# Kernel tuning notes

Hardware: AMD Instinct MI355X
Metric: run time of the kernel (lower is better)

Reference implementation:

```python
import jax, jax.numpy as jnp
import numpy as np
import math

B, N, D, H = 2, 64, 256, 8
DK = D // H


def setup_inputs() -> dict:
    key = jax.random.key(0)
    ks = jax.random.split(key, 12)
    s = 1.0 / math.sqrt(D)
    inp = {
        "state": jax.random.normal(ks[0], (B, N, N, D), dtype=jnp.float32),
        "mask": jnp.zeros((B, N, N, N), dtype=bool),
        "W_lk": jax.random.normal(ks[1], (D, D), dtype=jnp.float32) * s,
        "b_lk": jnp.zeros((D,), dtype=jnp.float32),
        "W_rk": jax.random.normal(ks[2], (D, D), dtype=jnp.float32) * s,
        "b_rk": jnp.zeros((D,), dtype=jnp.float32),
        "W_lv": jax.random.normal(ks[3], (D, D), dtype=jnp.float32) * s,
        "b_lv": jnp.zeros((D,), dtype=jnp.float32),
        "W_rv": jax.random.normal(ks[4], (D, D), dtype=jnp.float32) * s,
        "b_rv": jnp.zeros((D,), dtype=jnp.float32),
        "W_o": jax.random.normal(ks[5], (D, D), dtype=jnp.float32) * s,
        "b_o": jnp.zeros((D,), dtype=jnp.float32),
    }
    return inp


def _proj(x, W, b):
    # torch nn.Linear: x @ W.T + b, then view to heads
    y = jnp.einsum('bxyd,ed->bxye', x, W) + b
    return y.reshape(B, N, N, H, DK)


def reference(state, mask, W_lk, b_lk, W_rk, b_rk, W_lv, b_lv, W_rv, b_rv, W_o, b_o):
    left_k = _proj(state, W_lk, b_lk)   # [B,N,N,H,DK]
    right_k = _proj(state, W_rk, b_rk)
    left_v = _proj(state, W_lv, b_lv)
    right_v = _proj(state, W_rv, b_rv)

    # triangle-style scores over node triples (x, a, y): [B,N,N,N,H]
    scores = jnp.einsum('bxahd,bayhd->bxayh', left_k, right_k) / math.sqrt(DK)
    scores = jnp.where(mask[..., None], jnp.float32(-1000.0), scores)
    att = jax.nn.softmax(scores, axis=2)  # softmax over intermediate node a

    # val[b,x,a,y,h,d] = left_v[b,x,a,h,d] * right_v[b,a,y,h,d] (materialized as in torch)
    val = jnp.einsum('bxahd,bayhd->bxayhd', left_v, right_v)
    x = jnp.einsum('bxayh,bxayhd->bxyhd', att, val)  # sum over a
    x = x.reshape(B, N, N, D)
    return jnp.einsum('bxyd,ed->bxye', x, W_o) + b_o
```

## Files before the change

kernel.cpp:

```cpp
#include <hip/hip_runtime.h>

#define B 2
#define N 64
#define D 256
#define H 8
#define DK 32
#define M (B * N * N)

typedef __attribute__((ext_vector_type(8))) short bf16x8;
typedef __attribute__((ext_vector_type(4))) float f32x4;
typedef __attribute__((ext_vector_type(2))) float f32x2;

#define PROJ_ELEMS (2097152)

__device__ __forceinline__ ushort f2b(float f) {
    union { float f; unsigned u; } v; v.f = f;
    unsigned r = v.u + 0x7fffu + ((v.u >> 16) & 1u);
    return (ushort)(r >> 16);
}
__device__ __forceinline__ float b2f(ushort u) {
    union { unsigned u; float f; } v; v.u = ((unsigned)u) << 16; return v.f;
}
__device__ __forceinline__ f32x2 up2(unsigned u) {
    union { unsigned u; float f; } lo, hi;
    lo.u = u << 16; hi.u = u & 0xffff0000u;
    f32x2 r; r.x = lo.f; r.y = hi.f; return r;
}

__device__ __forceinline__ void glds16(const ushort* g, ushort* l) {
    __builtin_amdgcn_global_load_lds(
        (const __attribute__((address_space(1))) unsigned int*)g,
        (__attribute__((address_space(3))) unsigned int*)l, 16, 0, 0);
}

__global__ __launch_bounds__(256) void cast_all(const float* __restrict__ state,
                                                const float* __restrict__ W_lk, const float* __restrict__ W_rk,
                                                const float* __restrict__ W_lv, const float* __restrict__ W_rv,
                                                const float* __restrict__ W_o,
                                                const float* __restrict__ b_lk, const float* __restrict__ b_rk,
                                                const float* __restrict__ b_lv, const float* __restrict__ b_rv,
                                                const float* __restrict__ b_o,
                                                ushort* __restrict__ state_bf,
                                                ushort* __restrict__ Wcat,
                                                float* __restrict__ bias_cat) {
    const int gid = blockIdx.x * 256 + threadIdx.x;
    const float* Ws[5] = {W_lk, W_rk, W_lv, W_rv, W_o};
    const float* bs[5] = {b_lk, b_rk, b_lv, b_rv, b_o};

    if (gid < 1280) bias_cat[gid] = bs[gid >> 8][gid & 255];

    if (gid < 524288) {
        float4 v = *(const float4*)&state[(size_t)gid * 4];
        ushort4 o = {f2b(v.x), f2b(v.y), f2b(v.z), f2b(v.w)};
        *(ushort4*)&state_bf[(size_t)gid * 4] = o;
    } else {
        int u = gid - 524288;
        int row = u >> 6;
        int k4 = (u & 63) * 4;
        const float* W = Ws[row >> 8];
        float4 v = *(const float4*)&W[(size_t)(row & 255) * 256 + k4];
        ushort4 o = {f2b(v.x), f2b(v.y), f2b(v.z), f2b(v.w)};
        *(ushort4*)&Wcat[(size_t)row * 256 + k4] = o;
    }
}

template <int BF16OUT, int RELAYOUT, int BM>
__global__ __launch_bounds__(256) void gemm_mfma(const ushort* __restrict__ A,
                                                 const ushort* __restrict__ Bw,
                                                 const float* __restrict__ bias,
                                                 void* __restrict__ Cv, int ldc) {
    constexpr int IR = BM / 32;
    __shared__ __align__(16) ushort As[2][2][BM * 32];
    __shared__ __align__(16) ushort Bs[2][2][128 * 32];
    const int tid = threadIdx.x;
    const int lane = tid & 63;
    const int wave = tid >> 6;
    const int wm = (wave & 1) * (BM / 2);
    const int wn = (wave >> 1) * 64;
    const int row0 = blockIdx.x * BM;
    const int col0 = blockIdx.y * 128;

    const int lr = lane >> 2;
    const int lkq = (lane & 3) * 8;

    const int arow = (BM == 128) ? (wave * 32) : (wave * 16);
    const ushort* gA0 = A + (size_t)(row0 + arow + lr) * 256 + lkq;
    const ushort* gA1 = gA0 + 16 * 256;
    const ushort* gB0 = Bw + (size_t)(col0 + wave * 32 + lr) * 256 + lkq;
    const ushort* gB1 = gB0 + 16 * 256;

    const int fr = lane & 15;
    const int fk = (lane >> 4) * 8;

    f32x4 acc[IR][4] = {};

    auto stage2 = [&](int grp) {
        const int buf = grp & 1;
#pragma unroll
        for (int p = 0; p < 2; ++p) {
            const int ko = (grp * 2 + p) * 32;
            glds16(gA0 + ko, &As[buf][p][arow * 32]);
            if (BM == 128) glds16(gA1 + ko, &As[buf][p][(arow + 16) * 32]);
            glds16(gB0 + ko, &Bs[buf][p][(wave * 32) * 32]);
            glds16(gB1 + ko, &Bs[buf][p][(wave * 32 + 16) * 32]);
        }
    };

    stage2(0);
    __syncthreads();

    for (int it = 0; it < 4; ++it) {
        if (it < 3) stage2(it + 1);
        const int buf = it & 1;
#pragma unroll
        for (int p = 0; p < 2; ++p) {
            bf16x8 af[IR], bf[4];
#pragma unroll
            for (int i = 0; i < IR; ++i)
                af[i] = *(const bf16x8*)&As[buf][p][(wm + i * 16 + fr) * 32 + fk];
#pragma unroll
            for (int j = 0; j < 4; ++j)
                bf[j] = *(const bf16x8*)&Bs[buf][p][(wn + j * 16 + fr) * 32 + fk];
#pragma unroll
            for (int i = 0; i < IR; ++i)
#pragma unroll
                for (int j = 0; j < 4; ++j)
                    acc[i][j] = __builtin_amdgcn_mfma_f32_16x16x32_bf16(af[i], bf[j], acc[i][j], 0, 0, 0);
        }
        __syncthreads();
    }

#pragma unroll
    for (int j = 0; j < 4; ++j) {
        const int col = col0 + wn + j * 16 + (lane & 15);
        const float bv = bias[col];
#pragma unroll
        for (int i = 0; i < IR; ++i) {
            const int rbase = row0 + wm + i * 16 + (lane >> 4) * 4;
#pragma unroll
            for (int r = 0; r < 4; ++r) {
                float o = acc[i][j][r] + bv;
                if (RELAYOUT) {
                    const int row = rbase + r;
                    const int bb = row >> 12, rr = row & 4095;
                    const int proj = col >> 8, hh = (col >> 5) & 7, dk = col & 31;
                    ((ushort*)Cv)[(size_t)proj * PROJ_ELEMS +
                                  ((size_t)(bb * 8 + hh) * 4096 + rr) * 32 + dk] = f2b(o);
                } else if (BF16OUT) {
                    ((ushort*)Cv)[(size_t)(rbase + r) * ldc + col] = f2b(o);
                } else {
                    ((float*)Cv)[(size_t)(rbase + r) * ldc + col] = o;
                }
            }
        }
    }
}

__global__ __launch_bounds__(512, 2) void fused_attn(const ushort* __restrict__ P,
                                                     const unsigned char* __restrict__ mask,
                                                     ushort* __restrict__ xbuf) {
    __shared__ __align__(16) ushort LVb[16 * 1024];
    __shared__ __align__(16) ushort RVb[32 * 512];
    __shared__ __align__(16) float atts[32 * 16 * 20];
    __shared__ float mstate[16 * 20];
    __shared__ float alphas[16 * 20];

    const int bh = blockIdx.z;
    const int b = bh >> 3, h = bh & 7;
    const int x0 = blockIdx.x * 16, y0 = blockIdx.y * 16;
    const int tid = threadIdx.x;
    const int lane = tid & 63, wave = tid >> 6;

    const size_t HB = (size_t)bh * 4096 * 32;
    const ushort* PLK = P + HB;
    const ushort* PRK = P + (size_t)1 * PROJ_ELEMS + HB;
    const ushort* PLV = P + (size_t)2 * PROJ_ELEMS + HB;
    const ushort* PRV = P + (size_t)3 * PROJ_ELEMS + HB;

    const int gy = lane >> 2;
    const int du = lane & 3;
    const int sx = tid >> 4, sy = tid & 15;
    if (tid < 256) mstate[sx * 20 + sy] = -3.0e38f;

    const int sa = lane >> 2, soct = lane & 3;
    const int r2 = wave * 2;
    const int a4 = wave * 4;

    f32x2 acc[2][4] = {};
    float lacc[2] = {0.0f, 0.0f};
    const float scale = 0.17677669529663687f;

    for (int c = 0; c < 2; ++c) {
        const int ac = c * 32;
        __syncthreads();

        glds16(PLV + ((size_t)(x0 + r2) * 64 + ac + sa) * 32 + soct * 8,
               &LVb[r2 * 1024]);
        glds16(PLV + ((size_t)(x0 + r2) * 64 + ac + 16 + sa) * 32 + soct * 8,
               &LVb[r2 * 1024 + 512]);
        glds16(PLV + ((size_t)(x0 + r2 + 1) * 64 + ac + sa) * 32 + soct * 8,
               &LVb[(r2 + 1) * 1024]);
        glds16(PLV + ((size_t)(x0 + r2 + 1) * 64 + ac + 16 + sa) * 32 + soct * 8,
               &LVb[(r2 + 1) * 1024 + 512]);
#pragma unroll
        for (int k = 0; k < 4; ++k)
            glds16(PRV + ((size_t)(ac + a4 + k) * 64 + y0 + sa) * 32 + soct * 8,
                   &RVb[(a4 + k) * 512]);

        {
            const int fr = lane & 15, fk = (lane >> 4) * 8;
            const int yq = lane & 15, xq = (lane >> 4) * 4;
#pragma unroll
            for (int aw = 0; aw < 4; ++aw) {
                const int a = wave * 4 + aw;
                bf16x8 af = *(const bf16x8*)&PLK[((size_t)(x0 + fr) * 64 + ac + a) * 32 + fk];
                bf16x8 bf = *(const bf16x8*)&PRK[((size_t)(ac + a) * 64 + y0 + fr) * 32 + fk];
                f32x4 s = {};
                s = __builtin_amdgcn_mfma_f32_16x16x32_bf16(af, bf, s, 0, 0, 0);
#pragma unroll
                for (int rr = 0; rr < 4; ++rr) {
                    const int x = xq + rr;
                    float sv = s[rr] * scale;
                    if (mask[((size_t)(b * N + x0 + x) * N + ac + a) * N + y0 + yq]) sv = -1000.0f;
                    atts[(a * 16 + x) * 20 + yq] = sv;
                }
            }
        }
        __syncthreads();

        if (tid < 256) {
            float mc = -3.0e38f;
#pragma unroll
            for (int a = 0; a < 32; ++a) mc = fmaxf(mc, atts[(a * 16 + sx) * 20 + sy]);
            const float mold = mstate[sx * 20 + sy];
            const float mnew = fmaxf(mold, mc);
            mstate[sx * 20 + sy] = mnew;
            alphas[sx * 20 + sy] = __expf(mold - mnew);
        }
        __syncthreads();

        float mn[2];
#pragma unroll
        for (int i = 0; i < 2; ++i) {
            const int x = wave * 2 + i;
            const float av = alphas[x * 20 + gy];
            mn[i] = mstate[x * 20 + gy];
            lacc[i] *= av;
#pragma unroll
            for (int q = 0; q < 4; ++q) acc[i][q] *= av;
        }

        {
            const unsigned* LV32 = (const unsigned*)LVb;
            const unsigned* RV32 = (const unsigned*)RVb;
#pragma unroll
            for (int a = 0; a < 32; ++a) {
                const uint4 rvw = *(const uint4*)&RV32[a * 256 + gy * 16 + du * 4];
                const f32x2 rv0 = up2(rvw.x), rv1 = up2(rvw.y);
                const f32x2 rv2 = up2(rvw.z), rv3 = up2(rvw.w);
#pragma unroll
                for (int i = 0; i < 2; ++i) {
                    const int x = wave * 2 + i;
                    const uint4 lvw = *(const uint4*)&LV32[x * 512 + a * 16 + du * 4];
                    const float sv = atts[(a * 16 + x) * 20 + gy];
                    const float w = __expf(sv - mn[i]);
                    lacc[i] += w;
                    acc[i][0] += (up2(lvw.x) * w) * rv0;
                    acc[i][1] += (up2(lvw.y) * w) * rv1;
                    acc[i][2] += (up2(lvw.z) * w) * rv2;
                    acc[i][3] += (up2(lvw.w) * w) * rv3;
                }
            }
        }
    }

#pragma unroll
    for (int i = 0; i < 2; ++i) {
        const int x = wave * 2 + i;
        const float il = 1.0f / lacc[i];
        ushort o[8] __attribute__((aligned(16)));
#pragma unroll
        for (int q = 0; q < 4; ++q) {
            o[2 * q]     = f2b(acc[i][q].x * il);
            o[2 * q + 1] = f2b(acc[i][q].y * il);
        }
        *(uint4*)&xbuf[(((size_t)b * N + x0 + x) * N + y0 + gy) * D + h * DK + du * 8] =
            *(const uint4*)o;
    }
}

extern "C" void kernel_launch(void* const* d_in, const int* in_sizes, int n_in,
                              void* d_out, int out_size, void* d_ws, size_t ws_size,
                              hipStream_t stream) {
    const float* state = (const float*)d_in[0];
    const unsigned char* mask = (const unsigned char*)d_in[1];
    const float* W_lk = (const float*)d_in[2];
    const float* b_lk = (const float*)d_in[3];
    const float* W_rk = (const float*)d_in[4];
    const float* b_rk = (const float*)d_in[5];
    const float* W_lv = (const float*)d_in[6];
    const float* b_lv = (const float*)d_in[7];
    const float* W_rv = (const float*)d_in[8];
    const float* b_rv = (const float*)d_in[9];
    const float* W_o = (const float*)d_in[10];
    const float* b_o = (const float*)d_in[11];
    float* out = (float*)d_out;

    char* ws = (char*)d_ws;
    ushort* P_bf = (ushort*)ws;
    ws += (size_t)4 * PROJ_ELEMS * 2;
    float* bias_cat = (float*)ws;
    ws += 1280 * 4;
    ushort* state_bf = (ushort*)ws;
    ws += (size_t)M * D * 2;
    ushort* Wcat = (ushort*)ws;
    ws += (size_t)1280 * 256 * 2;
    ushort* xbuf_bf = (ushort*)ws;

    cast_all<<<2368, 256, 0, stream>>>(state, W_lk, W_rk, W_lv, W_rv, W_o,
                                       b_lk, b_rk, b_lv, b_rv, b_o,
                                       state_bf, Wcat, bias_cat);
    gemm_mfma<1, 1, 128><<<dim3(M / 128, 8), 256, 0, stream>>>(state_bf, Wcat, bias_cat, P_bf, 1024);
    fused_attn<<<dim3(4, 4, B * H), 512, 0, stream>>>(P_bf, mask, xbuf_bf);
    gemm_mfma<0, 0, 64><<<dim3(M / 64, 2), 256, 0, stream>>>(xbuf_bf, Wcat + 1024 * 256, bias_cat + 1024, out, 256);
}
```

Measured before the change: 124.0 us.

## Load left values directly into registers with prefetch and transpose score tile

Drops the shared-memory staging buffer for left values. Each thread now reads its own left-value rows from global memory into registers, with a four-deep software prefetch inside the accumulation loop. The score tile in shared memory is transposed so the MFMA output is stored as one float4, and the two per-thread weights are read as a float2. This cuts LDS traffic and footprint, which may raise occupancy, but the accumulation loop now depends on global load latency and more registers are in use.

```diff
diff --git a/kernel.cpp b/kernel.cpp
--- a/kernel.cpp
+++ b/kernel.cpp
@@ -159,7 +159,6 @@
 __global__ __launch_bounds__(512, 2) void fused_attn(const ushort* __restrict__ P,
                                                      const unsigned char* __restrict__ mask,
                                                      ushort* __restrict__ xbuf) {
-    __shared__ __align__(16) ushort LVb[16 * 1024];
     __shared__ __align__(16) ushort RVb[32 * 512];
     __shared__ __align__(16) float atts[32 * 16 * 20];
     __shared__ float mstate[16 * 20];
@@ -183,8 +182,10 @@
     if (tid < 256) mstate[sx * 20 + sy] = -3.0e38f;
 
     const int sa = lane >> 2, soct = lane & 3;
-    const int r2 = wave * 2;
     const int a4 = wave * 4;
+
+    const ushort* lvb0 = PLV + ((size_t)(x0 + wave * 2) * 64) * 32 + du * 8;
+    const ushort* lvb1 = lvb0 + 64 * 32;
 
     f32x2 acc[2][4] = {};
     float lacc[2] = {0.0f, 0.0f};
@@ -194,18 +195,17 @@
         const int ac = c * 32;
         __syncthreads();
 
-        glds16(PLV + ((size_t)(x0 + r2) * 64 + ac + sa) * 32 + soct * 8,
-               &LVb[r2 * 1024]);
-        glds16(PLV + ((size_t)(x0 + r2) * 64 + ac + 16 + sa) * 32 + soct * 8,
-               &LVb[r2 * 1024 + 512]);
-        glds16(PLV + ((size_t)(x0 + r2 + 1) * 64 + ac + sa) * 32 + soct * 8,
-               &LVb[(r2 + 1) * 1024]);
-        glds16(PLV + ((size_t)(x0 + r2 + 1) * 64 + ac + 16 + sa) * 32 + soct * 8,
-               &LVb[(r2 + 1) * 1024 + 512]);
 #pragma unroll
         for (int k = 0; k < 4; ++k)
             glds16(PRV + ((size_t)(ac + a4 + k) * 64 + y0 + sa) * 32 + soct * 8,
                    &RVb[(a4 + k) * 512]);
+
+        uint4 lvp[4][2];
+#pragma unroll
+        for (int s = 0; s < 4; ++s) {
+            lvp[s][0] = *(const uint4*)(lvb0 + (ac + s) * 32);
+            lvp[s][1] = *(const uint4*)(lvb1 + (ac + s) * 32);
+        }
 
         {
             const int fr = lane & 15, fk = (lane >> 4) * 8;
@@ -217,13 +217,16 @@
                 bf16x8 bf = *(const bf16x8*)&PRK[((size_t)(ac + a) * 64 + y0 + fr) * 32 + fk];
                 f32x4 s = {};
                 s = __builtin_amdgcn_mfma_f32_16x16x32_bf16(af, bf, s, 0, 0, 0);
+                float4 ov;
+                float* op = (float*)&ov;
 #pragma unroll
                 for (int rr = 0; rr < 4; ++rr) {
-                    const int x = xq + rr;
                     float sv = s[rr] * scale;
-                    if (mask[((size_t)(b * N + x0 + x) * N + ac + a) * N + y0 + yq]) sv = -1000.0f;
-                    atts[(a * 16 + x) * 20 + yq] = sv;
+                    if (mask[((size_t)(b * N + x0 + xq + rr) * N + ac + a) * N + y0 + yq])
+                        sv = -1000.0f;
+                    op[rr] = sv;
                 }
+                *(float4*)&atts[(a * 16 + yq) * 20 + xq] = ov;
             }
         }
         __syncthreads();
@@ -231,7 +234,7 @@
         if (tid < 256) {
             float mc = -3.0e38f;
 #pragma unroll
-            for (int a = 0; a < 32; ++a) mc = fmaxf(mc, atts[(a * 16 + sx) * 20 + sy]);
+            for (int a = 0; a < 32; ++a) mc = fmaxf(mc, atts[(a * 16 + sy) * 20 + sx]);
             const float mold = mstate[sx * 20 + sy];
             const float mnew = fmaxf(mold, mc);
             mstate[sx * 20 + sy] = mnew;
@@ -251,25 +254,31 @@
         }
 
         {
-            const unsigned* LV32 = (const unsigned*)LVb;
             const unsigned* RV32 = (const unsigned*)RVb;
 #pragma unroll
             for (int a = 0; a < 32; ++a) {
+                const uint4 lv0 = lvp[a & 3][0];
+                const uint4 lv1 = lvp[a & 3][1];
+                if (a < 28) {
+                    lvp[a & 3][0] = *(const uint4*)(lvb0 + (ac + a + 4) * 32);
+                    lvp[a & 3][1] = *(const uint4*)(lvb1 + (ac + a + 4) * 32);
+                }
                 const uint4 rvw = *(const uint4*)&RV32[a * 256 + gy * 16 + du * 4];
+                const float2 w2 = *(const float2*)&atts[(a * 16 + gy) * 20 + wave * 2];
+                const float w0 = __expf(w2.x - mn[0]);
+                const float w1 = __expf(w2.y - mn[1]);
+                lacc[0] += w0;
+                lacc[1] += w1;
                 const f32x2 rv0 = up2(rvw.x), rv1 = up2(rvw.y);
                 const f32x2 rv2 = up2(rvw.z), rv3 = up2(rvw.w);
-#pragma unroll
-                for (int i = 0; i < 2; ++i) {
-                    const int x = wave * 2 + i;
-                    const uint4 lvw = *(const uint4*)&LV32[x * 512 + a * 16 + du * 4];
-                    const float sv = atts[(a * 16 + x) * 20 + gy];
-                    const float w = __expf(sv - mn[i]);
-                    lacc[i] += w;
-                    acc[i][0] += (up2(lvw.x) * w) * rv0;
-                    acc[i][1] += (up2(lvw.y) * w) * rv1;
-                    acc[i][2] += (up2(lvw.z) * w) * rv2;
-                    acc[i][3] += (up2(lvw.w) * w) * rv3;
-                }
+                acc[0][0] += (up2(lv0.x) * w0) * rv0;
+                acc[0][1] += (up2(lv0.y) * w0) * rv1;
+                acc[0][2] += (up2(lv0.z) * w0) * rv2;
+                acc[0][3] += (up2(lv0.w) * w0) * rv3;
+                acc[1][0] += (up2(lv1.x) * w1) * rv0;
+                acc[1][1] += (up2(lv1.y) * w1) * rv1;
+                acc[1][2] += (up2(lv1.z) * w1) * rv2;
+                acc[1][3] += (up2(lv1.w) * w1) * rv3;
             }
         }
     }
```

Measured after the change: 123.7 us. No clear change (-0.2%).
